# Performance work log

Measured on AMD Instinct MI355X. Metric: run time of the kernel, lower is better.

The kernel has to match this reference:

```python
import jax, jax.numpy as jnp
import numpy as np

N, E = 4096, 32768
NI, EI, D, EH = 64, 16, 64, 128
NUM_STEPS = 3


def setup_inputs() -> dict:
    key = jax.random.key(0)
    ks = jax.random.split(key, 24)

    def w(k, shape, fan_in):
        return (jax.random.normal(k, shape, jnp.float32) / np.float32(np.sqrt(fan_in)))

    return {
        "node_feats": jax.random.normal(ks[0], (N, NI), jnp.float32),
        "edge_attr": jax.random.normal(ks[1], (E, EI), jnp.float32),
        "edge_index": jax.random.randint(ks[2], (2, E), 0, N),
        # project_node_feats: Linear(NI -> D)
        "W_p": w(ks[3], (NI, D), NI), "b_p": jnp.zeros((D,), jnp.float32),
        # project_edge_feats: Linear(EI -> EH)
        "W_pe": w(ks[4], (EI, EH), EI), "b_pe": jnp.zeros((EH,), jnp.float32),
        # edge_network (NNConv nn): Linear(EH -> D*D)
        "W_nn": w(ks[5], (EH, D * D), EH), "b_nn": jnp.zeros((D * D,), jnp.float32),
        # NNConv root weight + bias
        "W_root": w(ks[6], (D, D), D), "b_conv": jnp.zeros((D,), jnp.float32),
        # GRU (single layer), gate order r, z, n as in torch
        "w_ih": w(ks[7], (D, 3 * D), D), "w_hh": w(ks[8], (D, 3 * D), D),
        "b_ih": jnp.zeros((3 * D,), jnp.float32), "b_hh": jnp.zeros((3 * D,), jnp.float32),
        # edge_update_network: Linear(EH+2D -> EH), Linear(EH -> EH)
        "W_eu1": w(ks[9], (EH + 2 * D, EH), EH + 2 * D), "b_eu1": jnp.zeros((EH,), jnp.float32),
        "W_eu2": w(ks[10], (EH, EH), EH), "b_eu2": jnp.zeros((EH,), jnp.float32),
    }


def reference(node_feats, edge_attr, edge_index, W_p, b_p, W_pe, b_pe,
              W_nn, b_nn, W_root, b_conv, w_ih, w_hh, b_ih, b_hh,
              W_eu1, b_eu1, W_eu2, b_eu2):
    relu = jax.nn.relu
    row, col = edge_index[0], edge_index[1]  # source, target
    n_nodes = node_feats.shape[0]
    d = W_root.shape[0]

    h = relu(node_feats @ W_p + b_p)          # (N, D) projected node feats
    hidden = h                                  # GRU hidden state
    e = relu(edge_attr @ W_pe + b_pe)          # (E, EH) projected edge feats

    for _ in range(NUM_STEPS):
        # NNConv: per-edge weight matrix from edge MLP (dropout=0 in eval)
        We = relu(e @ W_nn + b_nn).reshape(-1, d, d)      # (E, D, D)
        msg = jnp.einsum('ed,edf->ef', h[row], We)        # gather + per-edge matmul
        agg = jax.ops.segment_sum(msg, col, num_segments=n_nodes)  # scatter-add
        m = relu(agg + h @ W_root + b_conv)                # conv output + activation

        # GRU cell (torch gate order: r, z, n)
        gi = m @ w_ih + b_ih
        gh = hidden @ w_hh + b_hh
        ir, iz, i_n = jnp.split(gi, 3, axis=-1)
        hr, hz, h_n = jnp.split(gh, 3, axis=-1)
        r = jax.nn.sigmoid(ir + hr)
        z = jax.nn.sigmoid(iz + hz)
        ncand = jnp.tanh(i_n + r * h_n)
        hidden = (1.0 - z) * ncand + z * hidden
        h = hidden

        # edge update: cat(h[row], h[col], e) -> 2-layer MLP
        ei = jnp.concatenate([h[row], h[col], e], axis=1)
        e = relu(relu(ei @ W_eu1 + b_eu1) @ W_eu2 + b_eu2)

    return h, e
```

## Files before the change

### kernel.cpp

```cpp
#include <hip/hip_runtime.h>
#include <stdint.h>

typedef __attribute__((ext_vector_type(8))) _Float16 f16x8;
typedef __attribute__((ext_vector_type(4))) float f32x4;

#define N_NODES 4096
#define N_EDGES 32768

__device__ __forceinline__ float sigm(float x) { return 1.f / (1.f + __expf(-x)); }

__device__ __forceinline__ f16x8 packh8(const float* p) {
  f16x8 r;
#pragma unroll
  for (int i = 0; i < 8; ++i) r[i] = (_Float16)p[i];
  return r;
}

__global__ void zero_agg_kernel(float* __restrict__ agg) {
  agg[blockIdx.x * 256 + threadIdx.x] = 0.f;
}

__global__ void prep_wnnT(const float* __restrict__ Wnn,
                          _Float16* __restrict__ WnnT) {
  __shared__ float tile[128][33];
  const int t = threadIdx.x;
  const int nb = blockIdx.x * 32;
  for (int i = 0; i < 16; ++i) {
    int g = i * 256 + t;
    int k = g >> 5, j = g & 31;
    tile[k][j] = Wnn[(size_t)k * 4096 + nb + j];
  }
  __syncthreads();
  for (int i = 0; i < 16; ++i) {
    int g = i * 256 + t;
    int j = g >> 7, k = g & 127;
    WnnT[(size_t)(nb + j) * 128 + k] = (_Float16)tile[k][j];
  }
}

__global__ void prep_small(const float* __restrict__ We1,
                           const float* __restrict__ We2,
                           _Float16* __restrict__ We1T,
                           _Float16* __restrict__ We2T) {
  int idx = blockIdx.x * 256 + threadIdx.x;
  if (idx < 32768) {
    int n = idx >> 8, k = idx & 255;
    We1T[idx] = (_Float16)We1[(size_t)k * 128 + n];
  } else {
    int j = idx - 32768;
    int n = j >> 7, k = j & 127;
    We2T[j] = (_Float16)We2[(size_t)k * 128 + n];
  }
}

__global__ void proj_node_f(const float* __restrict__ nf,
                            const float* __restrict__ Wp,
                            const float* __restrict__ bp,
                            float* __restrict__ h) {
  int idx = blockIdx.x * 256 + threadIdx.x;
  int n = idx >> 6, c = idx & 63;
  float acc = bp[c];
  for (int k = 0; k < 64; ++k)
    acc = fmaf(nf[n * 64 + k], Wp[k * 64 + c], acc);
  h[idx] = fmaxf(acc, 0.f);
}

__launch_bounds__(256)
__global__ void proj_edge_f2(const float* __restrict__ ea,
                             const float* __restrict__ Wpe,
                             const float* __restrict__ bpe,
                             float* __restrict__ e) {
  __shared__ float sw[16 * 128];
  __shared__ float sb[128];
  __shared__ float sa[32][17];
  const int t = threadIdx.x;
  const int ebase = blockIdx.x * 32;
  for (int g = t; g < 2048; g += 256) sw[g] = Wpe[g];
  if (t < 128) sb[t] = bpe[t];
  for (int g = t; g < 512; g += 256) {
    int r = g >> 4, k = g & 15;
    sa[r][k] = ea[(size_t)(ebase + r) * 16 + k];
  }
  __syncthreads();
  int c = t & 127, eg = t >> 7;
  float wc[16];
#pragma unroll
  for (int k = 0; k < 16; ++k) wc[k] = sw[k * 128 + c];
  float bv = sb[c];
#pragma unroll
  for (int i = 0; i < 16; ++i) {
    int ee = eg * 16 + i;
    float acc = bv;
#pragma unroll
    for (int k = 0; k < 16; ++k) acc = fmaf(sa[ee][k], wc[k], acc);
    e[(size_t)(ebase + ee) * 128 + c] = fmaxf(acc, 0.f);
  }
}

__launch_bounds__(256, 2)
__global__ void fused_msg_m(const float* __restrict__ ebf,
                            const float* __restrict__ hid,
                            const _Float16* __restrict__ WnnT,
                            const float* __restrict__ bnn,
                            const int* __restrict__ eidx,
                            float* __restrict__ agg) {
  __shared__ float Hs[64 * 132];
  const int t = threadIdx.x;
  const int w = t >> 6, l = t & 63, l15 = l & 15, q = l >> 4;
  const int ebase = blockIdx.x * 128;

#pragma unroll
  for (int i = 0; i < 8; ++i) {
    int g = i * 256 + t;
    int e = g >> 4, d4 = g & 15;
    int r = eidx[ebase + e];
    float4 v = *(const float4*)&hid[(size_t)r * 64 + d4 * 4];
    Hs[(d4 * 4 + 0) * 132 + e] = v.x;
    Hs[(d4 * 4 + 1) * 132 + e] = v.y;
    Hs[(d4 * 4 + 2) * 132 + e] = v.z;
    Hs[(d4 * 4 + 3) * 132 + e] = v.w;
  }

  f16x8 af[8][4];
#pragma unroll
  for (int m = 0; m < 8; ++m)
#pragma unroll
    for (int kk = 0; kk < 4; ++kk)
      af[m][kk] = packh8(&ebf[(size_t)(ebase + m * 16 + l15) * 128 + kk * 32 + q * 8]);

  float msg[8][4];
#pragma unroll
  for (int m = 0; m < 8; ++m)
#pragma unroll
    for (int rr = 0; rr < 4; ++rr) msg[m][rr] = 0.f;

  __syncthreads();

  const _Float16* wb = WnnT + (size_t)(w * 16 + l15) * 128 + q * 8;
  f16x8 bb[4], nb[4];
#pragma unroll
  for (int kk = 0; kk < 4; ++kk) bb[kk] = *(const f16x8*)(wb + kk * 32);

  for (int d = 0; d < 64; ++d) {
    if (d < 63) {
      const _Float16* p = wb + (size_t)(d + 1) * 8192;
#pragma unroll
      for (int kk = 0; kk < 4; ++kk) nb[kk] = *(const f16x8*)(p + kk * 32);
    }
    float bnv = bnn[d * 64 + w * 16 + l15];
#pragma unroll
    for (int m = 0; m < 8; ++m) {
      f32x4 C = {0.f, 0.f, 0.f, 0.f};
#pragma unroll
      for (int kk = 0; kk < 4; ++kk)
        C = __builtin_amdgcn_mfma_f32_16x16x32_f16(af[m][kk], bb[kk], C, 0, 0, 0);
      float4 hv = *(const float4*)&Hs[d * 132 + m * 16 + q * 4];
      msg[m][0] = fmaf(hv.x, fmaxf(C[0] + bnv, 0.f), msg[m][0]);
      msg[m][1] = fmaf(hv.y, fmaxf(C[1] + bnv, 0.f), msg[m][1]);
      msg[m][2] = fmaf(hv.z, fmaxf(C[2] + bnv, 0.f), msg[m][2]);
      msg[m][3] = fmaf(hv.w, fmaxf(C[3] + bnv, 0.f), msg[m][3]);
    }
#pragma unroll
    for (int kk = 0; kk < 4; ++kk) bb[kk] = nb[kk];
  }

  const int* colp = eidx + N_EDGES;
#pragma unroll
  for (int m = 0; m < 8; ++m)
#pragma unroll
    for (int rr = 0; rr < 4; ++rr) {
      int col = colp[ebase + m * 16 + q * 4 + rr];
      atomicAdd(&agg[(size_t)col * 64 + w * 16 + l15], msg[m][rr]);
    }
}

__global__ void node_update_f(const float* __restrict__ agg,
                              float* __restrict__ hid,
                              const float* __restrict__ Wroot,
                              const float* __restrict__ bconv,
                              const float* __restrict__ wih,
                              const float* __restrict__ whh,
                              const float* __restrict__ bih,
                              const float* __restrict__ bhh) {
  __shared__ __align__(16) float sh[16 * 64];
  __shared__ __align__(16) float sm[16 * 64];
  __shared__ __align__(16) float sg[16 * 384];
  const int t = threadIdx.x;
  const int nb = blockIdx.x * 16;

  for (int i = 0; i < 4; ++i) sh[i * 256 + t] = hid[nb * 64 + i * 256 + t];
  __syncthreads();

  for (int i = 0; i < 4; ++i) {
    int idx = i * 256 + t;
    int nl = idx >> 6, dc = idx & 63;
    float acc = bconv[dc] + agg[nb * 64 + idx];
    for (int k = 0; k < 64; ++k)
      acc = fmaf(sh[nl * 64 + k], Wroot[k * 64 + dc], acc);
    sm[idx] = fmaxf(acc, 0.f);
  }
  __syncthreads();

  for (int i = 0; i < 24; ++i) {
    int idx = i * 256 + t;
    int nl = idx / 384, j2 = idx % 384;
    float acc;
    if (j2 < 192) {
      acc = bih[j2];
      for (int k = 0; k < 64; ++k)
        acc = fmaf(sm[nl * 64 + k], wih[k * 192 + j2], acc);
    } else {
      int j = j2 - 192;
      acc = bhh[j];
      for (int k = 0; k < 64; ++k)
        acc = fmaf(sh[nl * 64 + k], whh[k * 192 + j], acc);
    }
    sg[idx] = acc;
  }
  __syncthreads();

  for (int i = 0; i < 4; ++i) {
    int idx = i * 256 + t;
    int nl = idx >> 6, dc = idx & 63;
    const float* g = &sg[nl * 384];
    float ir = g[dc], iz = g[64 + dc], in_ = g[128 + dc];
    float hr = g[192 + dc], hz = g[256 + dc], hn = g[320 + dc];
    float r = sigm(ir + hr), z = sigm(iz + hz);
    float nc = tanhf(in_ + r * hn);
    hid[nb * 64 + idx] = (1.f - z) * nc + z * sh[nl * 64 + dc];
  }
}

__launch_bounds__(256)
__global__ void edge_mlp_m(const float* __restrict__ hid,
                           float* __restrict__ ebf,
                           const int* __restrict__ eidx,
                           const _Float16* __restrict__ We1T,
                           const float* __restrict__ be1,
                           const _Float16* __restrict__ We2T,
                           const float* __restrict__ be2) {
  __shared__ _Float16 As[64 * 264];
  __shared__ _Float16 Ts[64 * 136];
  const int t = threadIdx.x;
  const int w = t >> 6, l = t & 63, l15 = l & 15, q = l >> 4;
  const int mbase = blockIdx.x * 64;

  for (int g = t; g < 2048; g += 256) {
    int r = g >> 5, kg = g & 31;
    int e = mbase + r;
    const float* src;
    if (kg < 8)       src = &hid[(size_t)eidx[e] * 64 + kg * 8];
    else if (kg < 16) src = &hid[(size_t)eidx[N_EDGES + e] * 64 + (kg - 8) * 8];
    else              src = &ebf[(size_t)e * 128 + (kg - 16) * 8];
    *(f16x8*)&As[r * 264 + kg * 8] = packh8(src);
  }
  __syncthreads();

  f32x4 zero4 = {0.f, 0.f, 0.f, 0.f};
  f32x4 acc[4][2];
#pragma unroll
  for (int m = 0; m < 4; ++m)
#pragma unroll
    for (int nn = 0; nn < 2; ++nn) acc[m][nn] = zero4;

#pragma unroll
  for (int kc = 0; kc < 4; ++kc)
#pragma unroll
    for (int kk = 0; kk < 2; ++kk) {
      int ko = kc * 64 + kk * 32 + q * 8;
      f16x8 b0 = *(const f16x8*)(We1T + (size_t)(w * 32 + l15) * 256 + ko);
      f16x8 b1 = *(const f16x8*)(We1T + (size_t)(w * 32 + 16 + l15) * 256 + ko);
#pragma unroll
      for (int m = 0; m < 4; ++m) {
        f16x8 a = *(const f16x8*)&As[(m * 16 + l15) * 264 + ko];
        acc[m][0] = __builtin_amdgcn_mfma_f32_16x16x32_f16(a, b0, acc[m][0], 0, 0, 0);
        acc[m][1] = __builtin_amdgcn_mfma_f32_16x16x32_f16(a, b1, acc[m][1], 0, 0, 0);
      }
    }

#pragma unroll
  for (int m = 0; m < 4; ++m)
#pragma unroll
    for (int nn = 0; nn < 2; ++nn) {
      int col = w * 32 + nn * 16 + l15;
      float bv = be1[col];
#pragma unroll
      for (int rr = 0; rr < 4; ++rr) {
        int row = m * 16 + q * 4 + rr;
        Ts[row * 136 + col] = (_Float16)fmaxf(acc[m][nn][rr] + bv, 0.f);
      }
    }
  __syncthreads();

  f32x4 acc2[4][2];
#pragma unroll
  for (int m = 0; m < 4; ++m)
#pragma unroll
    for (int nn = 0; nn < 2; ++nn) acc2[m][nn] = zero4;

#pragma unroll
  for (int kc = 0; kc < 2; ++kc)
#pragma unroll
    for (int kk = 0; kk < 2; ++kk) {
      int ko = kc * 64 + kk * 32 + q * 8;
      f16x8 b0 = *(const f16x8*)(We2T + (size_t)(w * 32 + l15) * 128 + ko);
      f16x8 b1 = *(const f16x8*)(We2T + (size_t)(w * 32 + 16 + l15) * 128 + ko);
#pragma unroll
      for (int m = 0; m < 4; ++m) {
        f16x8 a = *(const f16x8*)&Ts[(m * 16 + l15) * 136 + ko];
        acc2[m][0] = __builtin_amdgcn_mfma_f32_16x16x32_f16(a, b0, acc2[m][0], 0, 0, 0);
        acc2[m][1] = __builtin_amdgcn_mfma_f32_16x16x32_f16(a, b1, acc2[m][1], 0, 0, 0);
      }
    }

#pragma unroll
  for (int m = 0; m < 4; ++m)
#pragma unroll
    for (int nn = 0; nn < 2; ++nn) {
      int col = w * 32 + nn * 16 + l15;
      float bv = be2[col];
#pragma unroll
      for (int rr = 0; rr < 4; ++rr) {
        int row = mbase + m * 16 + q * 4 + rr;
        ebf[(size_t)row * 128 + col] = fmaxf(acc2[m][nn][rr] + bv, 0.f);
      }
    }
}

extern "C" void kernel_launch(void* const* d_in, const int* in_sizes, int n_in,
                              void* d_out, int out_size, void* d_ws, size_t ws_size,
                              hipStream_t stream) {
  const float* nf    = (const float*)d_in[0];
  const float* ea    = (const float*)d_in[1];
  const int*   eidx  = (const int*)d_in[2];
  const float* Wp    = (const float*)d_in[3];
  const float* bp    = (const float*)d_in[4];
  const float* Wpe   = (const float*)d_in[5];
  const float* bpe   = (const float*)d_in[6];
  const float* Wnn   = (const float*)d_in[7];
  const float* bnn   = (const float*)d_in[8];
  const float* Wroot = (const float*)d_in[9];
  const float* bconv = (const float*)d_in[10];
  const float* wih   = (const float*)d_in[11];
  const float* whh   = (const float*)d_in[12];
  const float* bih   = (const float*)d_in[13];
  const float* bhh   = (const float*)d_in[14];
  const float* We1   = (const float*)d_in[15];
  const float* be1   = (const float*)d_in[16];
  const float* We2   = (const float*)d_in[17];
  const float* be2   = (const float*)d_in[18];

  float* hid = (float*)d_out;
  float* ebf = (float*)d_out + 4096 * 64;

  char* ws = (char*)d_ws;
  _Float16* WnnT = (_Float16*)(ws + 0);
  _Float16* We1T = (_Float16*)(ws + 1048576);
  _Float16* We2T = (_Float16*)(ws + 1114112);
  float*    agg  = (float*)(ws + 1146880);

  prep_wnnT<<<128, 256, 0, stream>>>(Wnn, WnnT);
  prep_small<<<192, 256, 0, stream>>>(We1, We2, We1T, We2T);
  proj_node_f<<<1024, 256, 0, stream>>>(nf, Wp, bp, hid);
  proj_edge_f2<<<1024, 256, 0, stream>>>(ea, Wpe, bpe, ebf);

  for (int s = 0; s < 3; ++s) {
    zero_agg_kernel<<<1024, 256, 0, stream>>>(agg);
    fused_msg_m<<<256, 256, 0, stream>>>(ebf, hid, WnnT, bnn, eidx, agg);
    node_update_f<<<256, 256, 0, stream>>>(agg, hid, Wroot, bconv,
                                           wih, whh, bih, bhh);
    edge_mlp_m<<<512, 256, 0, stream>>>(hid, ebf, eidx, We1T, be1, We2T, be2);
  }
}
```

Measured before the change: 509.3 us.

## Split message kernel edges across 8 waves, fuse agg zeroing and prep kernels

The fused message kernel now runs 512 threads per block: waves 0-3 and 4-7 each handle half of the 128 edges, which halves the per-thread A-fragment and accumulator registers. Each block still covers the same edges, so the WnnT weight stream is read by two waves per column group. Zeroing of agg moves into node_update, which clears each element right after reading it, so three zero-kernel launches disappear from the loop. The two weight-prep kernels are merged into one launch. The risks are fewer resident blocks per CU and duplicated weight loads.

```diff
diff --git a/kernel.cpp b/kernel.cpp
--- a/kernel.cpp
+++ b/kernel.cpp
@@ -20,36 +20,37 @@
   agg[blockIdx.x * 256 + threadIdx.x] = 0.f;
 }
 
-__global__ void prep_wnnT(const float* __restrict__ Wnn,
-                          _Float16* __restrict__ WnnT) {
+__global__ void prep_all(const float* __restrict__ Wnn,
+                         const float* __restrict__ We1,
+                         const float* __restrict__ We2,
+                         _Float16* __restrict__ WnnT,
+                         _Float16* __restrict__ We1T,
+                         _Float16* __restrict__ We2T) {
   __shared__ float tile[128][33];
-  const int t = threadIdx.x;
-  const int nb = blockIdx.x * 32;
-  for (int i = 0; i < 16; ++i) {
-    int g = i * 256 + t;
-    int k = g >> 5, j = g & 31;
-    tile[k][j] = Wnn[(size_t)k * 4096 + nb + j];
-  }
-  __syncthreads();
-  for (int i = 0; i < 16; ++i) {
-    int g = i * 256 + t;
-    int j = g >> 7, k = g & 127;
-    WnnT[(size_t)(nb + j) * 128 + k] = (_Float16)tile[k][j];
-  }
-}
-
-__global__ void prep_small(const float* __restrict__ We1,
-                           const float* __restrict__ We2,
-                           _Float16* __restrict__ We1T,
-                           _Float16* __restrict__ We2T) {
-  int idx = blockIdx.x * 256 + threadIdx.x;
-  if (idx < 32768) {
-    int n = idx >> 8, k = idx & 255;
-    We1T[idx] = (_Float16)We1[(size_t)k * 128 + n];
+  const int b = blockIdx.x, t = threadIdx.x;
+  if (b < 128) {
+    const int nb = b * 32;
+    for (int i = 0; i < 16; ++i) {
+      int g = i * 256 + t;
+      int k = g >> 5, j = g & 31;
+      tile[k][j] = Wnn[(size_t)k * 4096 + nb + j];
+    }
+    __syncthreads();
+    for (int i = 0; i < 16; ++i) {
+      int g = i * 256 + t;
+      int j = g >> 7, k = g & 127;
+      WnnT[(size_t)(nb + j) * 128 + k] = (_Float16)tile[k][j];
+    }
   } else {
-    int j = idx - 32768;
-    int n = j >> 7, k = j & 127;
-    We2T[j] = (_Float16)We2[(size_t)k * 128 + n];
+    int idx = (b - 128) * 256 + t;
+    if (idx < 32768) {
+      int n = idx >> 8, k = idx & 255;
+      We1T[idx] = (_Float16)We1[(size_t)k * 128 + n];
+    } else {
+      int j = idx - 32768;
+      int n = j >> 7, k = j & 127;
+      We2T[j] = (_Float16)We2[(size_t)k * 128 + n];
+    }
   }
 }
 
@@ -97,7 +98,7 @@
   }
 }
 
-__launch_bounds__(256, 2)
+__launch_bounds__(512, 1)
 __global__ void fused_msg_m(const float* __restrict__ ebf,
                             const float* __restrict__ hid,
                             const _Float16* __restrict__ WnnT,
@@ -107,11 +108,13 @@
   __shared__ float Hs[64 * 132];
   const int t = threadIdx.x;
   const int w = t >> 6, l = t & 63, l15 = l & 15, q = l >> 4;
+  const int fw = w & 3;
+  const int eh = w >> 2;
   const int ebase = blockIdx.x * 128;
 
 #pragma unroll
-  for (int i = 0; i < 8; ++i) {
-    int g = i * 256 + t;
+  for (int i = 0; i < 4; ++i) {
+    int g = i * 512 + t;
     int e = g >> 4, d4 = g & 15;
     int r = eidx[ebase + e];
     float4 v = *(const float4*)&hid[(size_t)r * 64 + d4 * 4];
@@ -121,22 +124,22 @@
     Hs[(d4 * 4 + 3) * 132 + e] = v.w;
   }
 
-  f16x8 af[8][4];
-#pragma unroll
-  for (int m = 0; m < 8; ++m)
+  f16x8 af[4][4];
+#pragma unroll
+  for (int m = 0; m < 4; ++m)
 #pragma unroll
     for (int kk = 0; kk < 4; ++kk)
-      af[m][kk] = packh8(&ebf[(size_t)(ebase + m * 16 + l15) * 128 + kk * 32 + q * 8]);
-
-  float msg[8][4];
-#pragma unroll
-  for (int m = 0; m < 8; ++m)
+      af[m][kk] = packh8(&ebf[(size_t)(ebase + eh * 64 + m * 16 + l15) * 128 + kk * 32 + q * 8]);
+
+  float msg[4][4];
+#pragma unroll
+  for (int m = 0; m < 4; ++m)
 #pragma unroll
     for (int rr = 0; rr < 4; ++rr) msg[m][rr] = 0.f;
 
   __syncthreads();
 
-  const _Float16* wb = WnnT + (size_t)(w * 16 + l15) * 128 + q * 8;
+  const _Float16* wb = WnnT + (size_t)(fw * 16 + l15) * 128 + q * 8;
   f16x8 bb[4], nb[4];
 #pragma unroll
   for (int kk = 0; kk < 4; ++kk) bb[kk] = *(const f16x8*)(wb + kk * 32);
@@ -147,14 +150,14 @@
 #pragma unroll
       for (int kk = 0; kk < 4; ++kk) nb[kk] = *(const f16x8*)(p + kk * 32);
     }
-    float bnv = bnn[d * 64 + w * 16 + l15];
-#pragma unroll
-    for (int m = 0; m < 8; ++m) {
+    float bnv = bnn[d * 64 + fw * 16 + l15];
+#pragma unroll
+    for (int m = 0; m < 4; ++m) {
       f32x4 C = {0.f, 0.f, 0.f, 0.f};
 #pragma unroll
       for (int kk = 0; kk < 4; ++kk)
         C = __builtin_amdgcn_mfma_f32_16x16x32_f16(af[m][kk], bb[kk], C, 0, 0, 0);
-      float4 hv = *(const float4*)&Hs[d * 132 + m * 16 + q * 4];
+      float4 hv = *(const float4*)&Hs[d * 132 + eh * 64 + m * 16 + q * 4];
       msg[m][0] = fmaf(hv.x, fmaxf(C[0] + bnv, 0.f), msg[m][0]);
       msg[m][1] = fmaf(hv.y, fmaxf(C[1] + bnv, 0.f), msg[m][1]);
       msg[m][2] = fmaf(hv.z, fmaxf(C[2] + bnv, 0.f), msg[m][2]);
@@ -166,15 +169,16 @@
 
   const int* colp = eidx + N_EDGES;
 #pragma unroll
-  for (int m = 0; m < 8; ++m)
+  for (int m = 0; m < 4; ++m)
 #pragma unroll
     for (int rr = 0; rr < 4; ++rr) {
-      int col = colp[ebase + m * 16 + q * 4 + rr];
-      atomicAdd(&agg[(size_t)col * 64 + w * 16 + l15], msg[m][rr]);
-    }
-}
-
-__global__ void node_update_f(const float* __restrict__ agg,
+      int col = colp[ebase + eh * 64 + m * 16 + q * 4 + rr];
+      atomicAdd(&agg[(size_t)col * 64 + fw * 16 + l15], msg[m][rr]);
+    }
+}
+
+__global__ void node_update_f(const float* __restrict__ agg_r,
+                              float* __restrict__ agg_w,
                               float* __restrict__ hid,
                               const float* __restrict__ Wroot,
                               const float* __restrict__ bconv,
@@ -194,7 +198,7 @@
   for (int i = 0; i < 4; ++i) {
     int idx = i * 256 + t;
     int nl = idx >> 6, dc = idx & 63;
-    float acc = bconv[dc] + agg[nb * 64 + idx];
+    float acc = bconv[dc] + agg_r[nb * 64 + idx];
     for (int k = 0; k < 64; ++k)
       acc = fmaf(sh[nl * 64 + k], Wroot[k * 64 + dc], acc);
     sm[idx] = fmaxf(acc, 0.f);
@@ -228,6 +232,7 @@
     float r = sigm(ir + hr), z = sigm(iz + hz);
     float nc = tanhf(in_ + r * hn);
     hid[nb * 64 + idx] = (1.f - z) * nc + z * sh[nl * 64 + dc];
+    agg_w[nb * 64 + idx] = 0.f;
   }
 }
 
@@ -359,15 +364,14 @@
   _Float16* We2T = (_Float16*)(ws + 1114112);
   float*    agg  = (float*)(ws + 1146880);
 
-  prep_wnnT<<<128, 256, 0, stream>>>(Wnn, WnnT);
-  prep_small<<<192, 256, 0, stream>>>(We1, We2, We1T, We2T);
+  prep_all<<<320, 256, 0, stream>>>(Wnn, We1, We2, WnnT, We1T, We2T);
   proj_node_f<<<1024, 256, 0, stream>>>(nf, Wp, bp, hid);
   proj_edge_f2<<<1024, 256, 0, stream>>>(ea, Wpe, bpe, ebf);
+  zero_agg_kernel<<<1024, 256, 0, stream>>>(agg);
 
   for (int s = 0; s < 3; ++s) {
-    zero_agg_kernel<<<1024, 256, 0, stream>>>(agg);
-    fused_msg_m<<<256, 256, 0, stream>>>(ebf, hid, WnnT, bnn, eidx, agg);
-    node_update_f<<<256, 256, 0, stream>>>(agg, hid, Wroot, bconv,
+    fused_msg_m<<<256, 512, 0, stream>>>(ebf, hid, WnnT, bnn, eidx, agg);
+    node_update_f<<<256, 256, 0, stream>>>(agg, agg, hid, Wroot, bconv,
                                            wih, whh, bih, bhh);
     edge_mlp_m<<<512, 256, 0, stream>>>(hid, ebf, eidx, We1T, be1, We2T, be2);
   }
```

Result: slower. 559.4 us (+9.8%).
